# Optimization experiments

Measured on AMD Instinct MI355X. Metric: run time of the kernel, lower is better.

Reference implementation:

```python
import jax, jax.numpy as jnp
import numpy as np

R = 0.2          # stable-distribution hash bucket width
TABLE_SIZE = 2   # hash table size (buckets)
M = 5            # number of appended ALSH transform dims
EPS = 1e-12


def conv2d(x, W, b, pad):
    out = jax.lax.conv_general_dilated(
        x, W, window_strides=(1, 1), padding=[(pad, pad), (pad, pad)],
        dimension_numbers=('NCHW', 'OIHW', 'NCHW'))
    return out + b[None, :, None, None]


def maxpool2(x):
    return jax.lax.reduce_window(x, -jnp.inf, jax.lax.max,
                                 (1, 1, 2, 2), (1, 1, 2, 2), 'VALID')


def alsh_mask(x, W, a, c):
    """ALSH filter selection: hash P(kernels) and Q(query) with a stable
    distribution hash h(v)=floor((a.v+b)/r) mod table_size; active filters
    are those landing in the query's bucket. Returns [B, Cout] 0/1 mask.
    Multiplying conv output by this mask == gather active filters then
    zero_fill_missing back to full channel count."""
    Cout, Cin, kH, kW = W.shape
    Kf = W.reshape(Cout, -1)                       # [Cout, Cin*kH*kW]
    norms = jnp.linalg.norm(Kf, axis=1)
    Kn = Kf / (jnp.max(norms) + EPS)               # scale so all norms <= 1
    n = jnp.linalg.norm(Kn, axis=1, keepdims=True)
    # P transform: append norm^2, norm^4, ..., norm^(2^M)
    powers = jnp.concatenate([n ** (2 ** (i + 1)) for i in range(M)], axis=1)
    P = jnp.concatenate([Kn, powers], axis=1)      # [Cout, d+M]
    kh = jnp.mod(jnp.floor((P @ a + c[0]) / R), TABLE_SIZE)  # [Cout]
    # query vector: per-sample channel means broadcast over kernel support
    cm = x.mean(axis=(2, 3))                       # [B, Cin]
    q = jnp.repeat(cm, kH * kW, axis=1)            # [B, Cin*kH*kW] (cin,kh,kw order)
    qn = q / (jnp.linalg.norm(q, axis=1, keepdims=True) + EPS)
    # Q transform: append M halves
    Qv = jnp.concatenate([qn, jnp.full((q.shape[0], M), 0.5, q.dtype)], axis=1)
    qh = jnp.mod(jnp.floor((Qv @ a + c[0]) / R), TABLE_SIZE)  # [B]
    return (kh[None, :] == qh[:, None]).astype(x.dtype)       # [B, Cout]


def setup_inputs() -> dict:
    key = jax.random.key(0)
    ks = jax.random.split(key, 16)
    u = lambda k, s: jax.random.uniform(k, s, jnp.float32, 0.0, R)
    n = lambda k, s, sc=0.1: jax.random.normal(k, s, jnp.float32) * sc
    return {
        'x': jax.random.normal(ks[0], (4096, 3, 32, 32), jnp.float32),
        'W1': n(ks[1], (16, 3, 5, 5)), 'b1': n(ks[2], (16,)),
        'a1': jax.random.normal(ks[3], (80,), jnp.float32), 'c1': u(ks[4], (1,)),
        'W2': n(ks[5], (20, 16, 5, 5)), 'b2': n(ks[6], (20,)),
        'a2': jax.random.normal(ks[7], (405,), jnp.float32), 'c2': u(ks[8], (1,)),
        'W3': n(ks[9], (20, 20, 5, 5)), 'b3': n(ks[10], (20,)),
        'a3': jax.random.normal(ks[11], (505,), jnp.float32), 'c3': u(ks[12], (1,)),
        'Wo': n(ks[13], (10, 320)), 'bo': n(ks[14], (10,)),
    }


def reference(x, W1, b1, a1, c1, W2, b2, a2, c2, W3, b3, a3, c3, Wo, bo):
    m1 = alsh_mask(x, W1, a1, c1)
    h = jax.nn.relu(conv2d(x, W1, b1, 2)) * m1[:, :, None, None]
    h = maxpool2(h)                                # [B,16,16,16]
    m2 = alsh_mask(h, W2, a2, c2)
    h = jax.nn.relu(conv2d(h, W2, b2, 2)) * m2[:, :, None, None]
    h = maxpool2(h)                                # [B,20,8,8]
    m3 = alsh_mask(h, W3, a3, c3)
    h = jax.nn.relu(conv2d(h, W3, b3, 2)) * m3[:, :, None, None]
    # zero_fill_missing -> identity here: inactive channels already zero
    h = maxpool2(h)                                # [B,20,4,4]
    flat = h.reshape(h.shape[0], -1)               # [B,320]
    return flat @ Wo.T + bo
```

## Files before the change

kernel.cpp:

```cpp
#include <hip/hip_runtime.h>
#include <hip/hip_bf16.h>

#define EPSV 1e-12
#define RHASH 0.2

__device__ __forceinline__ int fmod2(double t) {
    return (int)(((long long)floor(t)) & 1LL);
}

__device__ __forceinline__ void load_row6(const float* base, float* r) {
    float2 a0 = *(const float2*)(base);
    float2 a1 = *(const float2*)(base + 2);
    float2 a2 = *(const float2*)(base + 4);
    r[0] = a0.x; r[1] = a0.y; r[2] = a1.x; r[3] = a1.y; r[4] = a2.x; r[5] = a2.y;
}

__device__ __forceinline__ void load_row12(const float* base, float* r) {
    #pragma unroll
    for (int j = 0; j < 6; ++j) *(float2*)&r[2 * j] = *(const float2*)(base + 2 * j);
}

#define FMA8(c,kx,w) { float wg=(w); \
  acc[c][0]=fmaf(wg,ca[kx],acc[c][0]); acc[c][1]=fmaf(wg,ca[(kx)+1],acc[c][1]); \
  acc[c][2]=fmaf(wg,na[kx],acc[c][2]); acc[c][3]=fmaf(wg,na[(kx)+1],acc[c][3]); \
  acc[c][4]=fmaf(wg,cb[kx],acc[c][4]); acc[c][5]=fmaf(wg,cb[(kx)+1],acc[c][5]); \
  acc[c][6]=fmaf(wg,nb[kx],acc[c][6]); acc[c][7]=fmaf(wg,nb[(kx)+1],acc[c][7]); }

#define FMA4(c,kx,w) { float wg=(w); \
  acc[c][0]=fmaf(wg,cur[kx],acc[c][0]); acc[c][1]=fmaf(wg,cur[(kx)+1],acc[c][1]); \
  acc[c][2]=fmaf(wg,nxt[kx],acc[c][2]); acc[c][3]=fmaf(wg,nxt[(kx)+1],acc[c][3]); }

__device__ void layer_setup(const float* W, const float* a, double cval,
                            int Co, int Ci, int* kh, double* asum, double* qc,
                            double* s_norm, float* Wbuf, float* abuf)
{
    const int t = threadIdx.x;
    const int D = Ci * 25;
    for (int i = t; i < Co * D; i += 256) Wbuf[i] = W[i];
    for (int i = t; i < D + 5; i += 256) abuf[i] = a[i];
    __syncthreads();
    if (t < Co) {
        double s = 0;
        for (int j = 0; j < D; ++j) { double w = (double)Wbuf[t * D + j]; s += w * w; }
        s_norm[t] = sqrt(s);
    }
    __syncthreads();
    if (t == 0) {
        double mx = 0;
        for (int i = 0; i < Co; ++i) mx = fmax(mx, s_norm[i]);
        s_norm[23] = 1.0 / (mx + EPSV);
    }
    __syncthreads();
    double scale = s_norm[23];
    if (t < Co) {
        double dp = 0;
        for (int j = 0; j < D; ++j) dp += (double)Wbuf[t * D + j] * (double)abuf[j];
        dp *= scale;
        double n = s_norm[t] * scale;
        double p = n * n;
        for (int m = 0; m < 5; ++m) { dp += p * (double)abuf[D + m]; p *= p; }
        kh[t] = fmod2((dp + cval) / RHASH);
    }
    if (t >= 64 && t < 64 + Ci) {
        int c = t - 64;
        double s = 0;
        for (int j = 0; j < 25; ++j) s += (double)abuf[c * 25 + j];
        asum[c] = s;
    }
    if (t == 128) {
        double s = 0;
        for (int m = 0; m < 5; ++m) s += (double)abuf[D + m];
        *qc = 0.5 * s + cval;
    }
    __syncthreads();
}

__global__ __launch_bounds__(256) void setup_kernel(
    const float* W1, const float* a1, const float* c1,
    const float* W2, const float* a2, const float* c2,
    const float* W3, const float* a3, const float* c3,
    double* dmeta, int* imeta)
{
    __shared__ float Wbuf[10000];
    __shared__ float abuf[512];
    __shared__ double s_norm[24];
    layer_setup(W1, a1, (double)c1[0], 16, 3,  imeta + 0,  dmeta + 0,  dmeta + 39, s_norm, Wbuf, abuf);
    layer_setup(W2, a2, (double)c2[0], 20, 16, imeta + 16, dmeta + 3,  dmeta + 40, s_norm, Wbuf, abuf);
    layer_setup(W3, a3, (double)c3[0], 20, 20, imeta + 36, dmeta + 19, dmeta + 41, s_norm, Wbuf, abuf);
}

__global__ __launch_bounds__(256) void pack_kernel(const float* W1, const float* W2, const float* W3,
                                                   float* Wp1, float* Wp2, float* Wp3)
{
    int i = blockIdx.x * 256 + threadIdx.x;
    if (i < 1200) {
        int co = i & 15, r = i >> 4;
        int kx = r % 5, r2 = r / 5, ky = r2 % 5, ci = r2 / 5;
        Wp1[i] = W1[co * 75 + ci * 25 + ky * 5 + kx];
    } else if (i < 1200 + 8960) {
        int k = i - 1200;
        int j = k % 28, r = k / 28;
        int cog = r % 4, r2 = r / 4, ky = r2 % 5, ci = r2 / 5;
        Wp2[k] = (j < 25) ? W2[(cog * 5 + j / 5) * 400 + ci * 25 + ky * 5 + (j % 5)] : 0.f;
    } else if (i < 1200 + 8960 + 11200) {
        int k = i - 10160;
        int j = k % 28, r = k / 28;
        int cog = r % 4, r2 = r / 4, ky = r2 % 5, ci = r2 / 5;
        Wp3[k] = (j < 25) ? W3[(cog * 5 + j / 5) * 500 + ci * 25 + ky * 5 + (j % 5)] : 0.f;
    }
}

__global__ __launch_bounds__(256) void conv1_kernel(
    const float* __restrict__ x, const float* __restrict__ Wp1,
    const float* __restrict__ b1, const int* __restrict__ kh1,
    const double* __restrict__ dmeta, float* __restrict__ h1,
    int* __restrict__ qh2)
{
    __shared__ float xs[3][36][36];
    __shared__ float Ws[1200];
    __shared__ double s_red[3];
    __shared__ double s_ch[16][4];

    const int b = blockIdx.x, t = threadIdx.x;
    const int w = t >> 6, ln = t & 63;

    for (int i = t; i < 3 * 36 * 36; i += 256) (&xs[0][0][0])[i] = 0.f;
    for (int i = t; i < 600; i += 256) ((float2*)Ws)[i] = ((const float2*)Wp1)[i];
    __syncthreads();
    const float2* xb2 = (const float2*)(x + (size_t)b * 3072);
    for (int i = t; i < 1536; i += 256) {
        int idx = i * 2, c = idx >> 10, rem = idx & 1023;
        *(float2*)&xs[c][(rem >> 5) + 2][(rem & 31) + 2] = xb2[i];
    }
    __syncthreads();

    if (w < 3) {
        double s = 0;
        for (int j = 0; j < 16; ++j) {
            int i = ln + 64 * j;
            s += (double)xs[w][(i >> 5) + 2][(i & 31) + 2];
        }
        #pragma unroll
        for (int off = 32; off; off >>= 1) s += __shfl_xor(s, off);
        if (ln == 0) s_red[w] = s;
    }
    __syncthreads();
    double dp = 0, nn = 0;
    #pragma unroll
    for (int c = 0; c < 3; ++c) {
        double cm = s_red[c] * (1.0 / 1024.0);
        dp += cm * dmeta[c]; nn += cm * cm;
    }
    const int qh = fmod2((dp / (5.0 * sqrt(nn) + EPSV) + dmeta[39]) / RHASH);

    const int cog = ln >> 5;
    const int py = 4 * w + ((ln >> 3) & 3), pxp = ln & 7;
    const int y0 = 2 * py, x0a = 2 * pxp, x0b = 2 * pxp + 16;

    float acc[8][8];
    #pragma unroll
    for (int c = 0; c < 8; ++c) {
        float bb = b1[cog * 8 + c];
        #pragma unroll
        for (int j = 0; j < 8; ++j) acc[c][j] = bb;
    }

    #pragma unroll
    for (int ci = 0; ci < 3; ++ci) {
        #pragma unroll
        for (int ky = 0; ky < 5; ++ky) {
            float ca[6], na[6], cb[6], nb[6];
            load_row6(&xs[ci][y0 + ky][x0a],     ca);
            load_row6(&xs[ci][y0 + ky + 1][x0a], na);
            load_row6(&xs[ci][y0 + ky][x0b],     cb);
            load_row6(&xs[ci][y0 + ky + 1][x0b], nb);
            const float4* wq = (const float4*)&Ws[((ci * 5 + ky) * 5) * 16 + cog * 8];
            #pragma unroll
            for (int kx = 0; kx < 5; ++kx) {
                float4 w0 = wq[kx * 4];
                float4 w1 = wq[kx * 4 + 1];
                FMA8(0, kx, w0.x) FMA8(1, kx, w0.y) FMA8(2, kx, w0.z) FMA8(3, kx, w0.w)
                FMA8(4, kx, w1.x) FMA8(5, kx, w1.y) FMA8(6, kx, w1.z) FMA8(7, kx, w1.w)
            }
        }
    }

    float* hb = h1 + (size_t)b * 4096 + py * 16 + pxp;
    double csum[8];
    #pragma unroll
    for (int c = 0; c < 8; ++c) {
        int co = cog * 8 + c;
        float mask = (kh1[co] == qh) ? 1.f : 0.f;
        float mA = fmaxf(fmaxf(acc[c][0], acc[c][1]), fmaxf(acc[c][2], acc[c][3]));
        float mB = fmaxf(fmaxf(acc[c][4], acc[c][5]), fmaxf(acc[c][6], acc[c][7]));
        float vA = fmaxf(mA, 0.f) * mask;
        float vB = fmaxf(mB, 0.f) * mask;
        hb[co * 256]     = vA;
        hb[co * 256 + 8] = vB;
        csum[c] = (double)vA + (double)vB;
    }
    #pragma unroll
    for (int c = 0; c < 8; ++c) {
        double s = csum[c];
        #pragma unroll
        for (int off = 16; off; off >>= 1) s += __shfl_xor(s, off);
        if ((ln & 31) == 0) s_ch[cog * 8 + c][w] = s;
    }
    __syncthreads();
    if (t == 0) {
        double dp2 = 0, nn2 = 0;
        #pragma unroll
        for (int c = 0; c < 16; ++c) {
            double cm = (s_ch[c][0] + s_ch[c][1] + s_ch[c][2] + s_ch[c][3]) * (1.0 / 256.0);
            dp2 += cm * dmeta[3 + c]; nn2 += cm * cm;
        }
        qh2[b] = fmod2((dp2 / (5.0 * sqrt(nn2) + EPSV) + dmeta[40]) / RHASH);
    }
}

__global__ __launch_bounds__(256) void conv2_kernel(
    const float* __restrict__ h1, const float* __restrict__ Wp2,
    const float* __restrict__ b2, const int* __restrict__ kh2,
    const int* __restrict__ qh2, const double* __restrict__ dmeta,
    float* __restrict__ h2, int* __restrict__ qh3, int B)
{
    __shared__ float xs[4][4][20][22];
    __shared__ float Ws[2240];
    __shared__ double s_ch[4][20];

    const int b0 = blockIdx.x * 4, t = threadIdx.x;
    const int s = t >> 6, l = t & 63;
    const int cog = l >> 4, pos = l & 15;
    const int py = pos >> 1, pxg = pos & 1;
    const int b = b0 + s;

    for (int i = t; i < 4 * 4 * 20 * 22; i += 256) (&xs[0][0][0][0])[i] = 0.f;

    const int qh = (b < B) ? qh2[b] : 0;
    float accA[5][8], accB[5][8];
    #pragma unroll
    for (int c = 0; c < 5; ++c) {
        float bb = b2[cog * 5 + c];
        #pragma unroll
        for (int k = 0; k < 8; ++k) { accA[c][k] = bb; accB[c][k] = bb; }
    }
    __syncthreads();

    for (int ch = 0; ch < 4; ++ch) {
        for (int i = t; i < 1120; i += 256)
            ((float2*)Ws)[i] = ((const float2*)(Wp2 + ch * 2240))[i];
        for (int i = t; i < 2048; i += 256) {
            int si = i >> 9, rem = i & 511, cil = rem >> 7, rr = rem & 127;
            int p2 = rr * 2, row = p2 >> 4, col = p2 & 15;
            if (b0 + si < B)
                *(float2*)&xs[si][cil][row + 2][col + 2] =
                    ((const float2*)(h1 + (size_t)(b0 + si) * 4096 + (size_t)(ch * 4 + cil) * 256))[rr];
        }
        __syncthreads();

        for (int cil = 0; cil < 4; ++cil) {
            float ra[12], rb[12];
            load_row12(&xs[s][cil][2 * py][8 * pxg],     ra);
            load_row12(&xs[s][cil][2 * py + 1][8 * pxg], rb);
            #pragma unroll
            for (int ky = 0; ky < 5; ++ky) {
                float wv[28];
                const float4* wp = (const float4*)&Ws[((cil * 5 + ky) * 4 + cog) * 28];
                *(float4*)&wv[0]  = wp[0];
                *(float4*)&wv[4]  = wp[1];
                *(float4*)&wv[8]  = wp[2];
                *(float4*)&wv[12] = wp[3];
                *(float4*)&wv[16] = wp[4];
                *(float4*)&wv[20] = wp[5];
                *(float4*)&wv[24] = wp[6];
                #pragma unroll
                for (int c = 0; c < 5; ++c) {
                    #pragma unroll
                    for (int kx = 0; kx < 5; ++kx) {
                        float wg = wv[c * 5 + kx];
                        #pragma unroll
                        for (int k = 0; k < 8; ++k) {
                            accA[c][k] = fmaf(wg, ra[k + kx], accA[c][k]);
                            accB[c][k] = fmaf(wg, rb[k + kx], accB[c][k]);
                        }
                    }
                }
                if (ky < 4) {
                    #pragma unroll
                    for (int j = 0; j < 12; ++j) ra[j] = rb[j];
                    load_row12(&xs[s][cil][2 * py + ky + 2][8 * pxg], rb);
                }
            }
        }
        __syncthreads();
    }

    float* ob = h2 + (size_t)b * 1280 + py * 8 + pxg * 4;
    double csum[5];
    #pragma unroll
    for (int c = 0; c < 5; ++c) {
        int co = cog * 5 + c;
        float mask = (kh2[co] == qh) ? 1.f : 0.f;
        float v0 = fmaxf(fmaxf(accA[c][0], accA[c][1]), fmaxf(accB[c][0], accB[c][1]));
        float v1 = fmaxf(fmaxf(accA[c][2], accA[c][3]), fmaxf(accB[c][2], accB[c][3]));
        float v2 = fmaxf(fmaxf(accA[c][4], accA[c][5]), fmaxf(accB[c][4], accB[c][5]));
        float v3 = fmaxf(fmaxf(accA[c][6], accA[c][7]), fmaxf(accB[c][6], accB[c][7]));
        v0 = fmaxf(v0, 0.f) * mask; v1 = fmaxf(v1, 0.f) * mask;
        v2 = fmaxf(v2, 0.f) * mask; v3 = fmaxf(v3, 0.f) * mask;
        if (b < B) *(float4*)(ob + co * 64) = make_float4(v0, v1, v2, v3);
        csum[c] = (double)v0 + (double)v1 + (double)v2 + (double)v3;
    }
    #pragma unroll
    for (int c = 0; c < 5; ++c) {
        double sv = csum[c];
        sv += __shfl_xor(sv, 8); sv += __shfl_xor(sv, 4);
        sv += __shfl_xor(sv, 2); sv += __shfl_xor(sv, 1);
        if (pos == 0) s_ch[s][cog * 5 + c] = sv;
    }
    __syncthreads();
    if (l == 0 && b < B) {
        double dp2 = 0, nn2 = 0;
        #pragma unroll
        for (int c = 0; c < 20; ++c) {
            double cm = s_ch[s][c] * (1.0 / 64.0);
            dp2 += cm * dmeta[19 + c]; nn2 += cm * cm;
        }
        qh3[b] = fmod2((dp2 / (5.0 * sqrt(nn2) + EPSV) + dmeta[41]) / RHASH);
    }
}

__global__ __launch_bounds__(256) void conv3_kernel(
    const float* __restrict__ h2, const float* __restrict__ Wp3,
    const float* __restrict__ b3, const int* __restrict__ kh3,
    const int* __restrict__ qh3,
    const float* __restrict__ Wo, const float* __restrict__ bo,
    float* __restrict__ out, int B)
{
    __shared__ float xs[4][5][12][12];
    __shared__ float Ws[2800];
    __shared__ float flat[4][320];

    const int b0 = blockIdx.x * 4, t = threadIdx.x;
    const int s = t >> 6, q0 = t & 63, cog = q0 >> 4, pos = q0 & 15;
    const int py = pos >> 2, px = pos & 3;
    const int y0 = 2 * py, x0 = 2 * px;
    const int b = b0 + s;

    for (int i = t; i < 4 * 5 * 144; i += 256) (&xs[0][0][0][0])[i] = 0.f;

    const int qh = (b < B) ? qh3[b] : 0;
    float acc[5][4];
    #pragma unroll
    for (int c = 0; c < 5; ++c) {
        float bb = b3[cog * 5 + c];
        acc[c][0] = bb; acc[c][1] = bb; acc[c][2] = bb; acc[c][3] = bb;
    }
    __syncthreads();

    for (int ch = 0; ch < 4; ++ch) {
        for (int i = t; i < 1400; i += 256)
            ((float2*)Ws)[i] = ((const float2*)(Wp3 + ch * 2800))[i];
        for (int i = t; i < 640; i += 256) {
            int ss = i / 160, r = i - ss * 160, ci = r >> 5, rr = r & 31, p2 = rr * 2;
            if (b0 + ss < B)
                *(float2*)&xs[ss][ci][(p2 >> 3) + 2][(p2 & 7) + 2] =
                    ((const float2*)(h2 + (size_t)(b0 + ss) * 1280 + (ch * 5 + ci) * 64))[rr];
        }
        __syncthreads();

        #pragma unroll
        for (int ci = 0; ci < 5; ++ci) {
            float cur[6], nxt[6];
            load_row6(&xs[s][ci][y0][x0], cur);
            load_row6(&xs[s][ci][y0 + 1][x0], nxt);
            #pragma unroll
            for (int ky = 0; ky < 5; ++ky) {
                const float* wrow = &Ws[((ci * 5 + ky) * 4 + cog) * 28];
                const float4* wq = (const float4*)wrow;
                float4 q;
                q = wq[0]; FMA4(0, 0, q.x) FMA4(0, 1, q.y) FMA4(0, 2, q.z) FMA4(0, 3, q.w)
                q = wq[1]; FMA4(0, 4, q.x) FMA4(1, 0, q.y) FMA4(1, 1, q.z) FMA4(1, 2, q.w)
                q = wq[2]; FMA4(1, 3, q.x) FMA4(1, 4, q.y) FMA4(2, 0, q.z) FMA4(2, 1, q.w)
                q = wq[3]; FMA4(2, 2, q.x) FMA4(2, 3, q.y) FMA4(2, 4, q.z) FMA4(3, 0, q.w)
                q = wq[4]; FMA4(3, 1, q.x) FMA4(3, 2, q.y) FMA4(3, 3, q.z) FMA4(3, 4, q.w)
                q = wq[5]; FMA4(4, 0, q.x) FMA4(4, 1, q.y) FMA4(4, 2, q.z) FMA4(4, 3, q.w)
                FMA4(4, 4, wrow[24])
                if (ky < 4) {
                    #pragma unroll
                    for (int j = 0; j < 6; ++j) cur[j] = nxt[j];
                    load_row6(&xs[s][ci][y0 + ky + 2][x0], nxt);
                }
            }
        }
        __syncthreads();
    }

    #pragma unroll
    for (int c = 0; c < 5; ++c) {
        int co = cog * 5 + c;
        float m = fmaxf(fmaxf(acc[c][0], acc[c][1]), fmaxf(acc[c][2], acc[c][3]));
        flat[s][co * 16 + pos] = fmaxf(m, 0.f) * ((kh3[co] == qh) ? 1.f : 0.f);
    }
    __syncthreads();

    if (t < 160) {
        const int g = t >> 2, qq = t & 3;
        const int ss = g / 10, o = g - ss * 10;
        float a = 0.f;
        const float* wr = Wo + o * 320;
        for (int k = qq; k < 320; k += 4) a = fmaf(flat[ss][k], wr[k], a);
        a += __shfl_xor(a, 1);
        a += __shfl_xor(a, 2);
        if (qq == 0 && b0 + ss < B) out[(size_t)(b0 + ss) * 10 + o] = a + bo[o];
    }
}

extern "C" void kernel_launch(void* const* d_in, const int* in_sizes, int n_in,
                              void* d_out, int out_size, void* d_ws, size_t ws_size,
                              hipStream_t stream)
{
    const float* x  = (const float*)d_in[0];
    const float* W1 = (const float*)d_in[1];
    const float* b1 = (const float*)d_in[2];
    const float* a1 = (const float*)d_in[3];
    const float* c1 = (const float*)d_in[4];
    const float* W2 = (const float*)d_in[5];
    const float* b2 = (const float*)d_in[6];
    const float* a2 = (const float*)d_in[7];
    const float* c2 = (const float*)d_in[8];
    const float* W3 = (const float*)d_in[9];
    const float* b3 = (const float*)d_in[10];
    const float* a3 = (const float*)d_in[11];
    const float* c3 = (const float*)d_in[12];
    const float* Wo = (const float*)d_in[13];
    const float* bo = (const float*)d_in[14];
    float* out = (float*)d_out;

    const int B = in_sizes[0] / 3072;

    float* h1  = (float*)d_ws;
    float* h2  = h1 + (size_t)B * 4096;
    float* Wp1 = h2 + (size_t)B * 1280;
    float* Wp2 = Wp1 + 1200;
    float* Wp3 = Wp2 + 8960;
    double* dmeta = (double*)(Wp3 + 11200);
    int* imeta = (int*)(dmeta + 42);
    int* qh2 = imeta + 56;
    int* qh3 = qh2 + B;

    setup_kernel<<<1, 256, 0, stream>>>(W1, a1, c1, W2, a2, c2, W3, a3, c3, dmeta, imeta);
    pack_kernel<<<84, 256, 0, stream>>>(W1, W2, W3, Wp1, Wp2, Wp3);
    conv1_kernel<<<B, 256, 0, stream>>>(x, Wp1, b1, imeta, dmeta, h1, qh2);
    conv2_kernel<<<(B + 3) / 4, 256, 0, stream>>>(h1, Wp2, b2, imeta + 16, qh2, dmeta, h2, qh3, B);
    conv3_kernel<<<(B + 3) / 4, 256, 0, stream>>>(h2, Wp3, b3, imeta + 36, qh3, Wo, bo, out, B);
}
```

Baseline: 523.1 us.

## Preload all conv2 weights and register-prefetch next input chunk per wave

The conv2 kernel now loads the whole weight tensor into shared memory once, instead of reloading it for each of the four input-channel chunks. Each wave now stages only its own sample's input tile, so the block-wide barriers between chunks are gone and the kernel relies on the wave executing in lockstep. While one chunk is being computed, the next chunk of input activations is prefetched into registers, overlapping global-memory latency with the FMAs. The cost is more shared memory per block (the weight buffer grows fourfold), which may lower occupancy, and extra registers for the double-buffered prefetch.

After: 537.4 us. 1.03x slower.

```diff
diff --git a/kernel.cpp b/kernel.cpp
--- a/kernel.cpp
+++ b/kernel.cpp
@@ -218,6 +218,57 @@
     }
 }
 
+#define C2_COMPUTE_CHUNK(CH)                                                  \
+    for (int cil = 0; cil < 4; ++cil) {                                       \
+        float ra[12], rb[12];                                                 \
+        load_row12(&xs[s][cil][2 * py][8 * pxg],     ra);                     \
+        load_row12(&xs[s][cil][2 * py + 1][8 * pxg], rb);                     \
+        _Pragma("unroll")                                                     \
+        for (int ky = 0; ky < 5; ++ky) {                                      \
+            float wv[28];                                                     \
+            const float4* wp = (const float4*)&Ws[((((CH) * 4 + cil) * 5 + ky) * 4 + cog) * 28]; \
+            *(float4*)&wv[0]  = wp[0];                                        \
+            *(float4*)&wv[4]  = wp[1];                                        \
+            *(float4*)&wv[8]  = wp[2];                                        \
+            *(float4*)&wv[12] = wp[3];                                        \
+            *(float4*)&wv[16] = wp[4];                                        \
+            *(float4*)&wv[20] = wp[5];                                        \
+            *(float4*)&wv[24] = wp[6];                                        \
+            _Pragma("unroll")                                                 \
+            for (int c = 0; c < 5; ++c) {                                     \
+                _Pragma("unroll")                                             \
+                for (int kx = 0; kx < 5; ++kx) {                              \
+                    float wg = wv[c * 5 + kx];                                \
+                    _Pragma("unroll")                                         \
+                    for (int k = 0; k < 8; ++k) {                             \
+                        accA[c][k] = fmaf(wg, ra[k + kx], accA[c][k]);        \
+                        accB[c][k] = fmaf(wg, rb[k + kx], accB[c][k]);        \
+                    }                                                         \
+                }                                                             \
+            }                                                                 \
+            if (ky < 4) {                                                     \
+                _Pragma("unroll")                                             \
+                for (int j = 0; j < 12; ++j) ra[j] = rb[j];                   \
+                load_row12(&xs[s][cil][2 * py + ky + 2][8 * pxg], rb);        \
+            }                                                                 \
+        }                                                                     \
+    }
+
+#define C2_COMMIT(RC)                                                         \
+    if (valid) {                                                              \
+        _Pragma("unroll")                                                     \
+        for (int j = 0; j < 8; ++j) {                                         \
+            int i = l + 64 * j, cil = i >> 7, rr = i & 127, p2 = rr * 2;      \
+            *(float2*)&xs[s][cil][(p2 >> 4) + 2][(p2 & 15) + 2] = RC[j];      \
+        }                                                                     \
+    }
+
+#define C2_PREFETCH(CH, RN)                                                   \
+    if (valid) {                                                              \
+        _Pragma("unroll")                                                     \
+        for (int j = 0; j < 8; ++j) RN[j] = hsrc[((CH) + 1) * 512 + l + 64 * j]; \
+    }
+
 __global__ __launch_bounds__(256) void conv2_kernel(
     const float* __restrict__ h1, const float* __restrict__ Wp2,
     const float* __restrict__ b2, const int* __restrict__ kh2,
@@ -225,7 +276,7 @@
     float* __restrict__ h2, int* __restrict__ qh3, int B)
 {
     __shared__ float xs[4][4][20][22];
-    __shared__ float Ws[2240];
+    __shared__ float Ws[8960];
     __shared__ double s_ch[4][20];
 
     const int b0 = blockIdx.x * 4, t = threadIdx.x;
@@ -233,10 +284,12 @@
     const int cog = l >> 4, pos = l & 15;
     const int py = pos >> 1, pxg = pos & 1;
     const int b = b0 + s;
-
-    for (int i = t; i < 4 * 4 * 20 * 22; i += 256) (&xs[0][0][0][0])[i] = 0.f;
-
-    const int qh = (b < B) ? qh2[b] : 0;
+    const bool valid = (b < B);
+
+    for (int i = t; i < 4480; i += 256) ((float2*)Ws)[i] = ((const float2*)Wp2)[i];
+    for (int i = l; i < 4 * 20 * 22; i += 64) (&xs[s][0][0][0])[i] = 0.f;
+
+    const int qh = valid ? qh2[b] : 0;
     float accA[5][8], accB[5][8];
     #pragma unroll
     for (int c = 0; c < 5; ++c) {
@@ -244,56 +297,19 @@
         #pragma unroll
         for (int k = 0; k < 8; ++k) { accA[c][k] = bb; accB[c][k] = bb; }
     }
-    __syncthreads();
-
-    for (int ch = 0; ch < 4; ++ch) {
-        for (int i = t; i < 1120; i += 256)
-            ((float2*)Ws)[i] = ((const float2*)(Wp2 + ch * 2240))[i];
-        for (int i = t; i < 2048; i += 256) {
-            int si = i >> 9, rem = i & 511, cil = rem >> 7, rr = rem & 127;
-            int p2 = rr * 2, row = p2 >> 4, col = p2 & 15;
-            if (b0 + si < B)
-                *(float2*)&xs[si][cil][row + 2][col + 2] =
-                    ((const float2*)(h1 + (size_t)(b0 + si) * 4096 + (size_t)(ch * 4 + cil) * 256))[rr];
-        }
-        __syncthreads();
-
-        for (int cil = 0; cil < 4; ++cil) {
-            float ra[12], rb[12];
-            load_row12(&xs[s][cil][2 * py][8 * pxg],     ra);
-            load_row12(&xs[s][cil][2 * py + 1][8 * pxg], rb);
-            #pragma unroll
-            for (int ky = 0; ky < 5; ++ky) {
-                float wv[28];
-                const float4* wp = (const float4*)&Ws[((cil * 5 + ky) * 4 + cog) * 28];
-                *(float4*)&wv[0]  = wp[0];
-                *(float4*)&wv[4]  = wp[1];
-                *(float4*)&wv[8]  = wp[2];
-                *(float4*)&wv[12] = wp[3];
-                *(float4*)&wv[16] = wp[4];
-                *(float4*)&wv[20] = wp[5];
-                *(float4*)&wv[24] = wp[6];
-                #pragma unroll
-                for (int c = 0; c < 5; ++c) {
-                    #pragma unroll
-                    for (int kx = 0; kx < 5; ++kx) {
-                        float wg = wv[c * 5 + kx];
-                        #pragma unroll
-                        for (int k = 0; k < 8; ++k) {
-                            accA[c][k] = fmaf(wg, ra[k + kx], accA[c][k]);
-                            accB[c][k] = fmaf(wg, rb[k + kx], accB[c][k]);
-                        }
-                    }
-                }
-                if (ky < 4) {
-                    #pragma unroll
-                    for (int j = 0; j < 12; ++j) ra[j] = rb[j];
-                    load_row12(&xs[s][cil][2 * py + ky + 2][8 * pxg], rb);
-                }
-            }
-        }
-        __syncthreads();
-    }
+
+    const float2* hsrc = (const float2*)(h1 + (size_t)b * 4096);
+    float2 rx0[8], rx1[8];
+    if (valid) {
+        #pragma unroll
+        for (int j = 0; j < 8; ++j) rx0[j] = hsrc[l + 64 * j];
+    }
+    __syncthreads();
+
+    C2_COMMIT(rx0) C2_PREFETCH(0, rx1) C2_COMPUTE_CHUNK(0)
+    C2_COMMIT(rx1) C2_PREFETCH(1, rx0) C2_COMPUTE_CHUNK(1)
+    C2_COMMIT(rx0) C2_PREFETCH(2, rx1) C2_COMPUTE_CHUNK(2)
+    C2_COMMIT(rx1)                      C2_COMPUTE_CHUNK(3)
 
     float* ob = h2 + (size_t)b * 1280 + py * 8 + pxg * 4;
     double csum[5];
@@ -307,7 +323,7 @@
         float v3 = fmaxf(fmaxf(accA[c][6], accA[c][7]), fmaxf(accB[c][6], accB[c][7]));
         v0 = fmaxf(v0, 0.f) * mask; v1 = fmaxf(v1, 0.f) * mask;
         v2 = fmaxf(v2, 0.f) * mask; v3 = fmaxf(v3, 0.f) * mask;
-        if (b < B) *(float4*)(ob + co * 64) = make_float4(v0, v1, v2, v3);
+        if (valid) *(float4*)(ob + co * 64) = make_float4(v0, v1, v2, v3);
         csum[c] = (double)v0 + (double)v1 + (double)v2 + (double)v3;
     }
     #pragma unroll
@@ -318,7 +334,7 @@
         if (pos == 0) s_ch[s][cog * 5 + c] = sv;
     }
     __syncthreads();
-    if (l == 0 && b < B) {
+    if (l == 0 && valid) {
         double dp2 = 0, nn2 = 0;
         #pragma unroll
         for (int c = 0; c < 20; ++c) {
```

## Retile conv1 threads to 4 channels x 4 pooled pixels with rolling row reuse

Applied to the files above, without the earlier changes.

Conv1 threads now each compute 4 output channels over a strip of 4 adjacent pooled outputs (8 conv columns, two rows) instead of 8 channels over two separated pooled pixels. Input rows are loaded once as 12-wide registers and rolled down between ky steps, so each loaded row feeds two output rows. The input tile row is padded from 36 to 38 to change the LDS bank mapping, and outputs are written as float4. This cuts redundant LDS reads and store instructions, at the cost of more weight loads per FMA and different register pressure.

Measured after the change: 514.0 us. About the same (-1.7%).

```diff
diff --git a/kernel.cpp b/kernel.cpp
--- a/kernel.cpp
+++ b/kernel.cpp
@@ -19,12 +19,6 @@
     #pragma unroll
     for (int j = 0; j < 6; ++j) *(float2*)&r[2 * j] = *(const float2*)(base + 2 * j);
 }
-
-#define FMA8(c,kx,w) { float wg=(w); \
-  acc[c][0]=fmaf(wg,ca[kx],acc[c][0]); acc[c][1]=fmaf(wg,ca[(kx)+1],acc[c][1]); \
-  acc[c][2]=fmaf(wg,na[kx],acc[c][2]); acc[c][3]=fmaf(wg,na[(kx)+1],acc[c][3]); \
-  acc[c][4]=fmaf(wg,cb[kx],acc[c][4]); acc[c][5]=fmaf(wg,cb[(kx)+1],acc[c][5]); \
-  acc[c][6]=fmaf(wg,nb[kx],acc[c][6]); acc[c][7]=fmaf(wg,nb[(kx)+1],acc[c][7]); }
 
 #define FMA4(c,kx,w) { float wg=(w); \
   acc[c][0]=fmaf(wg,cur[kx],acc[c][0]); acc[c][1]=fmaf(wg,cur[(kx)+1],acc[c][1]); \
@@ -116,7 +110,7 @@
     const double* __restrict__ dmeta, float* __restrict__ h1,
     int* __restrict__ qh2)
 {
-    __shared__ float xs[3][36][36];
+    __shared__ float xs[3][36][38];
     __shared__ float Ws[1200];
     __shared__ double s_red[3];
     __shared__ double s_ch[16][4];
@@ -124,13 +118,14 @@
     const int b = blockIdx.x, t = threadIdx.x;
     const int w = t >> 6, ln = t & 63;
 
-    for (int i = t; i < 3 * 36 * 36; i += 256) (&xs[0][0][0])[i] = 0.f;
+    for (int i = t; i < 3 * 36 * 38; i += 256) (&xs[0][0][0])[i] = 0.f;
     for (int i = t; i < 600; i += 256) ((float2*)Ws)[i] = ((const float2*)Wp1)[i];
     __syncthreads();
     const float2* xb2 = (const float2*)(x + (size_t)b * 3072);
     for (int i = t; i < 1536; i += 256) {
-        int idx = i * 2, c = idx >> 10, rem = idx & 1023;
-        *(float2*)&xs[c][(rem >> 5) + 2][(rem & 31) + 2] = xb2[i];
+        int c = i >> 9, rem = i & 511;
+        int row = rem >> 4, col2 = rem & 15;
+        *(float2*)&xs[c][row + 2][col2 * 2 + 2] = xb2[i];
     }
     __syncthreads();
 
@@ -153,58 +148,75 @@
     }
     const int qh = fmod2((dp / (5.0 * sqrt(nn) + EPSV) + dmeta[39]) / RHASH);
 
-    const int cog = ln >> 5;
-    const int py = 4 * w + ((ln >> 3) & 3), pxp = ln & 7;
-    const int y0 = 2 * py, x0a = 2 * pxp, x0b = 2 * pxp + 16;
-
-    float acc[8][8];
-    #pragma unroll
-    for (int c = 0; c < 8; ++c) {
-        float bb = b1[cog * 8 + c];
-        #pragma unroll
-        for (int j = 0; j < 8; ++j) acc[c][j] = bb;
+    const int cog = ln >> 4;
+    const int py = 4 * w + ((ln >> 2) & 3), pxg = ln & 3;
+    const int y0 = 2 * py, x0 = 8 * pxg;
+
+    float accA[4][8], accB[4][8];
+    #pragma unroll
+    for (int c = 0; c < 4; ++c) {
+        float bb = b1[cog * 4 + c];
+        #pragma unroll
+        for (int k = 0; k < 8; ++k) { accA[c][k] = bb; accB[c][k] = bb; }
     }
 
     #pragma unroll
     for (int ci = 0; ci < 3; ++ci) {
+        float ra[12], rb[12];
+        load_row12(&xs[ci][y0][x0],     ra);
+        load_row12(&xs[ci][y0 + 1][x0], rb);
         #pragma unroll
         for (int ky = 0; ky < 5; ++ky) {
-            float ca[6], na[6], cb[6], nb[6];
-            load_row6(&xs[ci][y0 + ky][x0a],     ca);
-            load_row6(&xs[ci][y0 + ky + 1][x0a], na);
-            load_row6(&xs[ci][y0 + ky][x0b],     cb);
-            load_row6(&xs[ci][y0 + ky + 1][x0b], nb);
-            const float4* wq = (const float4*)&Ws[((ci * 5 + ky) * 5) * 16 + cog * 8];
+            const float4* wq = (const float4*)&Ws[((ci * 5 + ky) * 5) * 16 + cog * 4];
             #pragma unroll
             for (int kx = 0; kx < 5; ++kx) {
-                float4 w0 = wq[kx * 4];
-                float4 w1 = wq[kx * 4 + 1];
-                FMA8(0, kx, w0.x) FMA8(1, kx, w0.y) FMA8(2, kx, w0.z) FMA8(3, kx, w0.w)
-                FMA8(4, kx, w1.x) FMA8(5, kx, w1.y) FMA8(6, kx, w1.z) FMA8(7, kx, w1.w)
+                float4 wv = wq[kx * 4];
+                { float wg = wv.x;
+                  #pragma unroll
+                  for (int k = 0; k < 8; ++k) { accA[0][k] = fmaf(wg, ra[k + kx], accA[0][k]);
+                                                accB[0][k] = fmaf(wg, rb[k + kx], accB[0][k]); } }
+                { float wg = wv.y;
+                  #pragma unroll
+                  for (int k = 0; k < 8; ++k) { accA[1][k] = fmaf(wg, ra[k + kx], accA[1][k]);
+                                                accB[1][k] = fmaf(wg, rb[k + kx], accB[1][k]); } }
+                { float wg = wv.z;
+                  #pragma unroll
+                  for (int k = 0; k < 8; ++k) { accA[2][k] = fmaf(wg, ra[k + kx], accA[2][k]);
+                                                accB[2][k] = fmaf(wg, rb[k + kx], accB[2][k]); } }
+                { float wg = wv.w;
+                  #pragma unroll
+                  for (int k = 0; k < 8; ++k) { accA[3][k] = fmaf(wg, ra[k + kx], accA[3][k]);
+                                                accB[3][k] = fmaf(wg, rb[k + kx], accB[3][k]); } }
             }
-        }
-    }
-
-    float* hb = h1 + (size_t)b * 4096 + py * 16 + pxp;
-    double csum[8];
-    #pragma unroll
-    for (int c = 0; c < 8; ++c) {
-        int co = cog * 8 + c;
+            if (ky < 4) {
+                #pragma unroll
+                for (int j = 0; j < 12; ++j) ra[j] = rb[j];
+                load_row12(&xs[ci][y0 + ky + 2][x0], rb);
+            }
+        }
+    }
+
+    float* hb = h1 + (size_t)b * 4096 + py * 16 + pxg * 4;
+    double csum[4];
+    #pragma unroll
+    for (int c = 0; c < 4; ++c) {
+        int co = cog * 4 + c;
         float mask = (kh1[co] == qh) ? 1.f : 0.f;
-        float mA = fmaxf(fmaxf(acc[c][0], acc[c][1]), fmaxf(acc[c][2], acc[c][3]));
-        float mB = fmaxf(fmaxf(acc[c][4], acc[c][5]), fmaxf(acc[c][6], acc[c][7]));
-        float vA = fmaxf(mA, 0.f) * mask;
-        float vB = fmaxf(mB, 0.f) * mask;
-        hb[co * 256]     = vA;
-        hb[co * 256 + 8] = vB;
-        csum[c] = (double)vA + (double)vB;
-    }
-    #pragma unroll
-    for (int c = 0; c < 8; ++c) {
+        float v0 = fmaxf(fmaxf(accA[c][0], accA[c][1]), fmaxf(accB[c][0], accB[c][1]));
+        float v1 = fmaxf(fmaxf(accA[c][2], accA[c][3]), fmaxf(accB[c][2], accB[c][3]));
+        float v2 = fmaxf(fmaxf(accA[c][4], accA[c][5]), fmaxf(accB[c][4], accB[c][5]));
+        float v3 = fmaxf(fmaxf(accA[c][6], accA[c][7]), fmaxf(accB[c][6], accB[c][7]));
+        v0 = fmaxf(v0, 0.f) * mask; v1 = fmaxf(v1, 0.f) * mask;
+        v2 = fmaxf(v2, 0.f) * mask; v3 = fmaxf(v3, 0.f) * mask;
+        *(float4*)(hb + co * 256) = make_float4(v0, v1, v2, v3);
+        csum[c] = (double)v0 + (double)v1 + (double)v2 + (double)v3;
+    }
+    #pragma unroll
+    for (int c = 0; c < 4; ++c) {
         double s = csum[c];
-        #pragma unroll
-        for (int off = 16; off; off >>= 1) s += __shfl_xor(s, off);
-        if ((ln & 31) == 0) s_ch[cog * 8 + c][w] = s;
+        s += __shfl_xor(s, 8); s += __shfl_xor(s, 4);
+        s += __shfl_xor(s, 2); s += __shfl_xor(s, 1);
+        if ((ln & 15) == 0) s_ch[cog * 4 + c][w] = s;
     }
     __syncthreads();
     if (t == 0) {
```
